# Kernel optimization log

Measured on AMD Instinct MI355X. Metric: run time of the kernel, lower is better.

## Reference

```python
import jax, jax.numpy as jnp
import numpy as np

B, T, L, D = 4, 8, 512, 512
H, KD, VD = 8, 64, 64


def setup_inputs() -> dict:
    key = jax.random.key(0)
    ks = jax.random.split(key, 8)
    s = 0.05
    return {
        "queries": jax.random.normal(ks[0], (B, T, L, D), jnp.float32),
        "keys": jax.random.normal(ks[1], (B, T, L, D), jnp.float32),
        "values": jax.random.normal(ks[2], (B, T, L, D), jnp.float32),
        "attn_mask": jnp.ones((1, 1, 1, L, L), jnp.float32),
        "Wq": jax.random.normal(ks[3], (D, H, KD), jnp.float32) * s,
        "Wk": jax.random.normal(ks[4], (D, H, KD), jnp.float32) * s,
        "Wv": jax.random.normal(ks[5], (D, H, VD), jnp.float32) * s,
        "w_head": jax.random.normal(ks[6], (H,), jnp.float32),
        "tau": jnp.ones((1,), jnp.float32),
        "delta": jnp.zeros((1,), jnp.float32),
    }


def reference(queries, keys, values, attn_mask, Wq, Wk, Wv, w_head, tau, delta):
    # Projections: (b,t,l,d) x (d,h,e) -> (b,t,l,h,e)
    Q = jnp.einsum('btld,dhe->btlhe', queries, Wq)
    K = jnp.einsum('btld,dhe->btlhe', keys, Wk)
    V = jnp.einsum('btld,dhe->btlhe', values, Wv)
    scale = 1.0 / jnp.sqrt(jnp.asarray(KD, jnp.float32))
    # Full score tensor (b,t,h,l,s)
    scores = jnp.einsum('btlhe,btshe->bthls', Q, K)
    # de-stationary rescaling, then scale, then multiplicative mask
    scores = (scores * tau[0] + delta[0]) * scale
    scores = scores * attn_mask
    # Dropout(attn_dropout) before softmax is identity at inference
    p = jax.nn.softmax(scores, axis=-1)
    attn = jnp.einsum('bthls,btshe->bthle', p, V)
    # Per-head scalar weighted sum over heads: (b,t,h,l,e),(h)->(b,t,l,e)
    return jnp.einsum('bthle,h->btle', attn, w_head)
```

## Files before the change

### kernel.cpp

```cpp
#include <hip/hip_runtime.h>
#include <hip/hip_bf16.h>

typedef __bf16 bf16;
typedef __bf16 bf16x4 __attribute__((ext_vector_type(4)));
typedef __bf16 bf16x8 __attribute__((ext_vector_type(8)));
typedef float f32x4 __attribute__((ext_vector_type(4)));
typedef _Float16 half4 __attribute__((ext_vector_type(4)));


#if __has_builtin(__builtin_amdgcn_exp2f)
#define EXP2(x) __builtin_amdgcn_exp2f(x)
#else
#define EXP2(x) exp2f(x)
#endif

static __device__ __forceinline__ f32x4 mfma16(bf16x4 a, bf16x4 b, f32x4 c) {
#if __has_builtin(__builtin_amdgcn_mfma_f32_16x16x16bf16_1k)
    return __builtin_amdgcn_mfma_f32_16x16x16bf16_1k(a, b, c, 0, 0, 0);
#else
    asm("v_mfma_f32_16x16x16_bf16 %0, %1, %2, %0" : "+v"(c) : "v"(a), "v"(b));
    return c;
#endif
}

__global__ __launch_bounds__(256) void prep_kernel(const float* __restrict__ W0,
                                                   const float* __restrict__ W1,
                                                   const float* __restrict__ W2,
                                                   const float* __restrict__ maskf,
                                                   bf16* __restrict__ Wt,
                                                   bf16* __restrict__ Mp) {
    if (blockIdx.z == 3) {
        const int bid = blockIdx.y * 8 + blockIdx.x;
        const int t0 = bid * 256 + threadIdx.x;
        const float4* m4 = (const float4*)maskf;
#pragma unroll
        for (int j = 0; j < 4; ++j) {
            int idx = t0 + j * 16384;
            int q = idx >> 7;
            int sc = idx & 127;
            int cc = sc >> 4;
            int ns = (sc >> 2) & 3;
            int qd = sc & 3;
            float4 v = m4[idx];
            bf16x4 o;
            o[0] = (bf16)v.x; o[1] = (bf16)v.y; o[2] = (bf16)v.z; o[3] = (bf16)v.w;
            size_t off = ((((size_t)(q >> 4) * 8 + cc) * 4 + ns) * 4 + qd) * 64 +
                         (q & 15) * 4;
            *(bf16x4*)&Mp[off] = o;
        }
        return;
    }
    __shared__ float t[64][65];
    const float* W = (blockIdx.z == 0) ? W0 : (blockIdx.z == 1) ? W1 : W2;
    bf16* O = Wt + (size_t)blockIdx.z * 512 * 512;
    const int d0 = blockIdx.x * 64, n0 = blockIdx.y * 64;
    {
        int nl = threadIdx.x & 63, dg = threadIdx.x >> 6;
#pragma unroll
        for (int j = 0; j < 16; ++j) {
            int dl = dg + j * 4;
            t[nl][dl] = W[(size_t)(d0 + dl) * 512 + n0 + nl];
        }
    }
    __syncthreads();
    {
        int dl = threadIdx.x & 63, ng = threadIdx.x >> 6;
#pragma unroll
        for (int j = 0; j < 16; ++j) {
            int nl = ng + j * 4;
            O[(size_t)(n0 + nl) * 512 + d0 + dl] = (bf16)t[nl][dl];
        }
    }
}

__global__ __launch_bounds__(256) void proj_kernel(
    const float* __restrict__ Xq, const float* __restrict__ Xk,
    const float* __restrict__ Xv, const bf16* __restrict__ Wt,
    bf16* __restrict__ Qw, bf16* __restrict__ Kw, bf16* __restrict__ Vt) {
    __shared__ __align__(16) bf16 smem[18432];
    bf16* la = smem;
    bf16* lb = smem + 128 * 72;

    const float* X = (blockIdx.z == 0) ? Xq : (blockIdx.z == 1) ? Xk : Xv;
    const bf16* W  = Wt + (size_t)blockIdx.z * 512 * 512;
    bf16* Out      = (blockIdx.z == 0) ? Qw : (blockIdx.z == 1) ? Kw : Vt;

    const int tid = threadIdx.x, wave = tid >> 6, lane = tid & 63;
    const int quad = lane >> 4, lc = lane & 15;
    const int wm = wave & 1, wn = wave >> 1;
    const int bid = blockIdx.x + (blockIdx.y << 7);
    const int jj = bid >> 3;
    const int yy = jj & 3;
    const int xt = (bid & 7) * 16 + (jj >> 2);
    const int m0 = xt * 128, n0 = yy * 128;

    f32x4 acc[4][4];
#pragma unroll
    for (int ms = 0; ms < 4; ++ms)
#pragma unroll
        for (int ns = 0; ns < 4; ++ns) acc[ms][ns] = (f32x4){0.f, 0.f, 0.f, 0.f};

    const int ar = tid >> 4, ac = tid & 15;
    const int br = tid >> 3, bc = tid & 7;

    float4 xr[8];
    bf16x8 wr[4];
#pragma unroll
    for (int i = 0; i < 8; ++i)
        xr[i] = *(const float4*)&X[(size_t)(m0 + ar + i * 16) * 512 + ac * 4];
#pragma unroll
    for (int i = 0; i < 4; ++i)
        wr[i] = *(const bf16x8*)&W[(size_t)(n0 + br + i * 32) * 512 + bc * 8];

    for (int kb = 0; kb < 512; kb += 64) {
        __syncthreads();
#pragma unroll
        for (int i = 0; i < 8; ++i) {
            float4 x = xr[i];
            bf16x4 p;
            p[0] = (bf16)x.x; p[1] = (bf16)x.y; p[2] = (bf16)x.z; p[3] = (bf16)x.w;
            *(bf16x4*)&la[(ar + i * 16) * 72 + ac * 4] = p;
        }
#pragma unroll
        for (int i = 0; i < 4; ++i)
            *(bf16x8*)&lb[(br + i * 32) * 72 + bc * 8] = wr[i];
        __syncthreads();
        if (kb < 448) {
            int kn = kb + 64;
#pragma unroll
            for (int i = 0; i < 8; ++i)
                xr[i] = *(const float4*)&X[(size_t)(m0 + ar + i * 16) * 512 + kn + ac * 4];
#pragma unroll
            for (int i = 0; i < 4; ++i)
                wr[i] = *(const bf16x8*)&W[(size_t)(n0 + br + i * 32) * 512 + kn + bc * 8];
        }
#pragma unroll
        for (int kk = 0; kk < 2; ++kk) {
            bf16x8 af[4], bfr[4];
#pragma unroll
            for (int ms = 0; ms < 4; ++ms)
                af[ms] = *(bf16x8*)&la[(wm * 64 + ms * 16 + lc) * 72 + kk * 32 + quad * 8];
#pragma unroll
            for (int ns = 0; ns < 4; ++ns)
                bfr[ns] = *(bf16x8*)&lb[(wn * 64 + ns * 16 + lc) * 72 + kk * 32 + quad * 8];
#pragma unroll
            for (int ms = 0; ms < 4; ++ms)
#pragma unroll
                for (int ns = 0; ns < 4; ++ns)
                    acc[ms][ns] = __builtin_amdgcn_mfma_f32_16x16x32_bf16(
                        af[ms], bfr[ns], acc[ms][ns], 0, 0, 0);
        }
    }
    __syncthreads();
    bf16* lds_c = smem;
    if (blockIdx.z != 2) {
#pragma unroll
        for (int ms = 0; ms < 4; ++ms)
#pragma unroll
            for (int ns = 0; ns < 4; ++ns)
#pragma unroll
                for (int r = 0; r < 4; ++r)
                    lds_c[(wm * 64 + ms * 16 + quad * 4 + r) * 136 +
                          wn * 64 + ns * 16 + lc] = (bf16)acc[ms][ns][r];
    } else {
#pragma unroll
        for (int ms = 0; ms < 4; ++ms)
#pragma unroll
            for (int ns = 0; ns < 4; ++ns)
#pragma unroll
                for (int r = 0; r < 4; ++r)
                    lds_c[(wn * 64 + ns * 16 + lc) * 136 +
                          wm * 64 + ms * 16 + quad * 4 + r] = (bf16)acc[ms][ns][r];
    }
    __syncthreads();
    const int bt = m0 >> 9, l0 = m0 & 511;
    if (blockIdx.z != 2) {
        const int ec = tid & 7, rg = tid >> 3;
#pragma unroll
        for (int hc = 0; hc < 2; ++hc) {
            int h = (n0 >> 6) + hc;
#pragma unroll
            for (int p = 0; p < 4; ++p) {
                int row = rg + p * 32;
                bf16x8 v = *(bf16x8*)&lds_c[row * 136 + hc * 64 + ec * 8];
                *(bf16x8*)&Out[(((size_t)bt * 8 + h) * 512 + l0 + row) * 64 + ec * 8] = v;
            }
        }
    } else {
        const int rowp = lane >> 2, cc = lane & 3;
#pragma unroll
        for (int pr = 0; pr < 2; ++pr) {
            int row = wave * 32 + pr * 16 + rowp;
            int h = (n0 >> 6) + (row >> 6);
            int e = row & 63;
            bf16* dst = Out + (((size_t)bt * 8 + h) * 64 + e) * 512 + l0;
#pragma unroll
            for (int pc = 0; pc < 4; ++pc) {
                int mc = cc + pc * 4;
                *(bf16x8*)&dst[mc * 8] = *(bf16x8*)&lds_c[row * 136 + mc * 8];
            }
        }
    }
}

__global__ __launch_bounds__(256, 4) void attn_kernel(
    const bf16* __restrict__ Qw, const bf16* __restrict__ Kw,
    const bf16* __restrict__ Vt, const bf16* __restrict__ Mp,
    const float* __restrict__ w_head, const float* __restrict__ tau,
    const float* __restrict__ delta, float* __restrict__ out,
    void* __restrict__ opart, int mode) {
    __shared__ __align__(16) bf16 lds_k[2][64 * 72];
    __shared__ __align__(16) bf16 lds_vt[2][64 * 72];

    const int tid  = threadIdx.x;
    const int wave = tid >> 6;
    const int lane = tid & 63;
    const int quad = lane >> 4;
    const int lc   = lane & 15;
    const int b    = blockIdx.x;
    const int bth  = b & 255;
    const int qquad = b >> 8;
    const int bt   = bth >> 3;
    const int h    = bth & 7;

    const bf16* Qh  = Qw + (size_t)bth * (512 * 64);
    const bf16* Kh  = Kw + (size_t)bth * (512 * 64);
    const bf16* VtH = Vt + (size_t)bth * (512 * 64);

    const float L2E = 1.4426950408889634f;
    const float ts = tau[0] * 0.125f * L2E;
    const float ds = delta[0] * 0.125f * L2E;
    const float wh = w_head[h];

    const int q0 = qquad * 128 + wave * 32;
    const size_t mbA = (size_t)(q0 >> 4) * 8192 + lane * 4;
    const size_t mbB = mbA + 8192;

    bf16x8 qfA[2], qfB[2];
#pragma unroll
    for (int kk = 0; kk < 2; ++kk) {
        qfA[kk] = *(const bf16x8*)&Qh[(size_t)(q0 + lc) * 64 + kk * 32 + quad * 8];
        qfB[kk] = *(const bf16x8*)&Qh[(size_t)(q0 + 16 + lc) * 64 + kk * 32 + quad * 8];
    }

    f32x4 oA[4], oB[4];
#pragma unroll
    for (int ns = 0; ns < 4; ++ns) {
        oA[ns] = (f32x4){0.f, 0.f, 0.f, 0.f};
        oB[ns] = (f32x4){0.f, 0.f, 0.f, 0.f};
    }
    float lA = 0.f, lB = 0.f;

    const int srow = tid >> 3, scc = tid & 7;
    bf16x8 kr[2], vr[2];
    kr[0] = *(const bf16x8*)&Kh[(size_t)srow * 64 + scc * 8];
    kr[1] = *(const bf16x8*)&Kh[(size_t)(srow + 32) * 64 + scc * 8];
    vr[0] = *(const bf16x8*)&VtH[(size_t)srow * 512 + scc * 8];
    vr[1] = *(const bf16x8*)&VtH[(size_t)(srow + 32) * 512 + scc * 8];
    *(bf16x8*)&lds_k[0][srow * 72 + scc * 8] = kr[0];
    *(bf16x8*)&lds_k[0][(srow + 32) * 72 + scc * 8] = kr[1];
    *(bf16x8*)&lds_vt[0][srow * 72 + scc * 8] = vr[0];
    *(bf16x8*)&lds_vt[0][(srow + 32) * 72 + scc * 8] = vr[1];
    kr[0] = *(const bf16x8*)&Kh[(size_t)(64 + srow) * 64 + scc * 8];
    kr[1] = *(const bf16x8*)&Kh[(size_t)(64 + srow + 32) * 64 + scc * 8];
    vr[0] = *(const bf16x8*)&VtH[(size_t)srow * 512 + 64 + scc * 8];
    vr[1] = *(const bf16x8*)&VtH[(size_t)(srow + 32) * 512 + 64 + scc * 8];

    for (int c = 0; c < 8; ++c) {
        const int buf = c & 1;
        __syncthreads();
        bf16x4 mA[4], mB[4];
        {
            const size_t mc = mbA + (size_t)c * 1024;
            const size_t md = mbB + (size_t)c * 1024;
#pragma unroll
            for (int ns = 0; ns < 4; ++ns) {
                mA[ns] = *(const bf16x4*)&Mp[mc + ns * 256];
                mB[ns] = *(const bf16x4*)&Mp[md + ns * 256];
            }
        }
        f32x4 stA[4], stB[4];
#pragma unroll
        for (int ns = 0; ns < 4; ++ns) {
            stA[ns] = (f32x4){0.f, 0.f, 0.f, 0.f};
            stB[ns] = (f32x4){0.f, 0.f, 0.f, 0.f};
        }
#pragma unroll
        for (int kk = 0; kk < 2; ++kk)
#pragma unroll
            for (int ns = 0; ns < 4; ++ns) {
                bf16x8 ka = *(bf16x8*)&lds_k[buf][(ns * 16 + lc) * 72 + kk * 32 + quad * 8];
                stA[ns] = __builtin_amdgcn_mfma_f32_16x16x32_bf16(ka, qfA[kk], stA[ns], 0, 0, 0);
                stB[ns] = __builtin_amdgcn_mfma_f32_16x16x32_bf16(ka, qfB[kk], stB[ns], 0, 0, 0);
            }
        if (c < 7) {
            const int nb = buf ^ 1;
            *(bf16x8*)&lds_k[nb][srow * 72 + scc * 8] = kr[0];
            *(bf16x8*)&lds_k[nb][(srow + 32) * 72 + scc * 8] = kr[1];
            *(bf16x8*)&lds_vt[nb][srow * 72 + scc * 8] = vr[0];
            *(bf16x8*)&lds_vt[nb][(srow + 32) * 72 + scc * 8] = vr[1];
            if (c < 6) {
                const int s0n = (c + 2) * 64;
                kr[0] = *(const bf16x8*)&Kh[(size_t)(s0n + srow) * 64 + scc * 8];
                kr[1] = *(const bf16x8*)&Kh[(size_t)(s0n + srow + 32) * 64 + scc * 8];
                vr[0] = *(const bf16x8*)&VtH[(size_t)srow * 512 + s0n + scc * 8];
                vr[1] = *(const bf16x8*)&VtH[(size_t)(srow + 32) * 512 + s0n + scc * 8];
            }
        }
        bf16x4 paA[4], paB[4];
#pragma unroll
        for (int ns = 0; ns < 4; ++ns) {
#pragma unroll
            for (int r = 0; r < 4; ++r) {
                float eA = (stA[ns][r] * ts + ds) * (float)mA[ns][r];
                float eB = (stB[ns][r] * ts + ds) * (float)mB[ns][r];
                float pA = EXP2(eA);
                float pB = EXP2(eB);
                lA += pA; lB += pB;
                paA[ns][r] = (bf16)pA;
                paB[ns][r] = (bf16)pB;
            }
        }
#pragma unroll
        for (int ks = 0; ks < 4; ++ks)
#pragma unroll
            for (int ns = 0; ns < 4; ++ns) {
                bf16x4 vv = *(bf16x4*)&lds_vt[buf][(ns * 16 + lc) * 72 + ks * 16 + quad * 4];
                oA[ns] = mfma16(paA[ks], vv, oA[ns]);
                oB[ns] = mfma16(paB[ks], vv, oB[ns]);
            }
    }
    lA += __shfl_xor(lA, 16, 64);
    lA += __shfl_xor(lA, 32, 64);
    lB += __shfl_xor(lB, 16, 64);
    lB += __shfl_xor(lB, 32, 64);
#pragma unroll
    for (int r = 0; r < 4; ++r) {
        float lrA = __shfl(lA, quad * 4 + r, 64);
        float lrB = __shfl(lB, quad * 4 + r, 64);
        float ivA = wh / lrA, ivB = wh / lrB;
        int qqA = q0 + quad * 4 + r;
        int qqB = q0 + 16 + quad * 4 + r;
        if (mode == 0) {
#pragma unroll
            for (int ns = 0; ns < 4; ++ns) {
                int e = ns * 16 + lc;
                atomicAdd(&out[((size_t)bt * 512 + qqA) * 64 + e], oA[ns][r] * ivA);
                atomicAdd(&out[((size_t)bt * 512 + qqB) * 64 + e], oB[ns][r] * ivB);
            }
        } else if (mode == 1) {
            float* op = (float*)opart;
#pragma unroll
            for (int ns = 0; ns < 4; ++ns) {
                int e = ns * 16 + lc;
                op[((size_t)bth * 512 + qqA) * 64 + e] = oA[ns][r] * ivA;
                op[((size_t)bth * 512 + qqB) * 64 + e] = oB[ns][r] * ivB;
            }
        } else {
            _Float16* op = (_Float16*)opart;
#pragma unroll
            for (int ns = 0; ns < 4; ++ns) {
                int e = ns * 16 + lc;
                op[((size_t)bth * 512 + qqA) * 64 + e] = (_Float16)(oA[ns][r] * ivA);
                op[((size_t)bth * 512 + qqB) * 64 + e] = (_Float16)(oB[ns][r] * ivB);
            }
        }
    }
}

__global__ __launch_bounds__(256) void reduce_kernel(const void* __restrict__ part,
                                                     float* __restrict__ out,
                                                     int mode) {
    const int idx = blockIdx.x * 256 + threadIdx.x;
    const int bt = idx >> 13;
    const int rf = idx & 8191;
    f32x4 s = (f32x4){0.f, 0.f, 0.f, 0.f};
    if (mode == 1) {
        const f32x4* p = (const f32x4*)part + (size_t)bt * 65536 + rf;
#pragma unroll
        for (int h = 0; h < 8; ++h) s += p[(size_t)h * 8192];
    } else {
        const half4* p = (const half4*)part + (size_t)bt * 65536 + rf;
#pragma unroll
        for (int h = 0; h < 8; ++h) {
            half4 v = p[(size_t)h * 8192];
            s[0] += (float)v[0]; s[1] += (float)v[1];
            s[2] += (float)v[2]; s[3] += (float)v[3];
        }
    }
    *(f32x4*)&out[(size_t)idx * 4] = s;
}

extern "C" void kernel_launch(void* const* d_in, const int* in_sizes, int n_in,
                              void* d_out, int out_size, void* d_ws, size_t ws_size,
                              hipStream_t stream) {
    const float* queries = (const float*)d_in[0];
    const float* keys    = (const float*)d_in[1];
    const float* values  = (const float*)d_in[2];
    const float* mask    = (const float*)d_in[3];
    const float* Wq      = (const float*)d_in[4];
    const float* Wk      = (const float*)d_in[5];
    const float* Wv      = (const float*)d_in[6];
    const float* w_head  = (const float*)d_in[7];
    const float* tau     = (const float*)d_in[8];
    const float* delta   = (const float*)d_in[9];

    char* ws = (char*)d_ws;
    bf16* Qw = (bf16*)(ws);
    bf16* Kw = (bf16*)(ws + 16777216ull);
    bf16* Vt = (bf16*)(ws + 33554432ull);
    bf16* Wt = (bf16*)(ws + 50331648ull);
    bf16* Mp = (bf16*)(ws + 51904512ull);
    char* Op = ws + 52428800ull;

    int mode = (ws_size >= 52428800ull + 33554432ull) ? 1
             : (ws_size >= 52428800ull + 16777216ull) ? 2 : 0;

    if (mode == 0)
        hipMemsetAsync(d_out, 0, (size_t)out_size * sizeof(float), stream);

    prep_kernel<<<dim3(8, 8, 4), 256, 0, stream>>>(Wq, Wk, Wv, mask, Wt, Mp);

    proj_kernel<<<dim3(128, 4, 3), 256, 0, stream>>>(queries, keys, values, Wt,
                                                     Qw, Kw, Vt);

    attn_kernel<<<1024, 256, 0, stream>>>(Qw, Kw, Vt, Mp, w_head, tau, delta,
                                          (float*)d_out, (void*)Op, mode);

    if (mode != 0)
        reduce_kernel<<<1024, 256, 0, stream>>>((const void*)Op, (float*)d_out,
                                                mode);
}
```

Measured before the change: 224.6 us.

## Double-buffer projection LDS, raise MFMA wave priority, and prefer mode 2 reduction

The projection GEMM now uses two LDS buffers, so the next k-chunk is converted and stored while the current one is consumed. This drops one barrier per iteration at the cost of doubling shared memory to 72 KB, which may lower occupancy. The attention kernel wraps its MFMA blocks in s_setprio to favour matrix issue across waves. The host no longer picks mode 1 and uses mode 2 partial-buffer reduction whenever the workspace allows, which changes the output reduction path.

```diff
diff --git a/kernel.cpp b/kernel.cpp
--- a/kernel.cpp
+++ b/kernel.cpp
@@ -77,9 +77,7 @@
     const float* __restrict__ Xq, const float* __restrict__ Xk,
     const float* __restrict__ Xv, const bf16* __restrict__ Wt,
     bf16* __restrict__ Qw, bf16* __restrict__ Kw, bf16* __restrict__ Vt) {
-    __shared__ __align__(16) bf16 smem[18432];
-    bf16* la = smem;
-    bf16* lb = smem + 128 * 72;
+    __shared__ __align__(16) bf16 smem[36864];
 
     const float* X = (blockIdx.z == 0) ? Xq : (blockIdx.z == 1) ? Xk : Xv;
     const bf16* W  = Wt + (size_t)blockIdx.z * 512 * 512;
@@ -111,28 +109,50 @@
 #pragma unroll
     for (int i = 0; i < 4; ++i)
         wr[i] = *(const bf16x8*)&W[(size_t)(n0 + br + i * 32) * 512 + bc * 8];
-
-    for (int kb = 0; kb < 512; kb += 64) {
+#pragma unroll
+    for (int i = 0; i < 8; ++i) {
+        float4 x = xr[i];
+        bf16x4 p;
+        p[0] = (bf16)x.x; p[1] = (bf16)x.y; p[2] = (bf16)x.z; p[3] = (bf16)x.w;
+        *(bf16x4*)&smem[(ar + i * 16) * 72 + ac * 4] = p;
+    }
+#pragma unroll
+    for (int i = 0; i < 4; ++i)
+        *(bf16x8*)&smem[9216 + (br + i * 32) * 72 + bc * 8] = wr[i];
+#pragma unroll
+    for (int i = 0; i < 8; ++i)
+        xr[i] = *(const float4*)&X[(size_t)(m0 + ar + i * 16) * 512 + 64 + ac * 4];
+#pragma unroll
+    for (int i = 0; i < 4; ++i)
+        wr[i] = *(const bf16x8*)&W[(size_t)(n0 + br + i * 32) * 512 + 64 + bc * 8];
+
+    for (int c = 0; c < 8; ++c) {
+        const int buf = c & 1;
+        bf16* la = smem + buf * 18432;
+        bf16* lb = la + 9216;
         __syncthreads();
-#pragma unroll
-        for (int i = 0; i < 8; ++i) {
-            float4 x = xr[i];
-            bf16x4 p;
-            p[0] = (bf16)x.x; p[1] = (bf16)x.y; p[2] = (bf16)x.z; p[3] = (bf16)x.w;
-            *(bf16x4*)&la[(ar + i * 16) * 72 + ac * 4] = p;
-        }
-#pragma unroll
-        for (int i = 0; i < 4; ++i)
-            *(bf16x8*)&lb[(br + i * 32) * 72 + bc * 8] = wr[i];
-        __syncthreads();
-        if (kb < 448) {
-            int kn = kb + 64;
-#pragma unroll
-            for (int i = 0; i < 8; ++i)
-                xr[i] = *(const float4*)&X[(size_t)(m0 + ar + i * 16) * 512 + kn + ac * 4];
+        if (c < 7) {
+            bf16* lan = smem + (buf ^ 1) * 18432;
+            bf16* lbn = lan + 9216;
+#pragma unroll
+            for (int i = 0; i < 8; ++i) {
+                float4 x = xr[i];
+                bf16x4 p;
+                p[0] = (bf16)x.x; p[1] = (bf16)x.y; p[2] = (bf16)x.z; p[3] = (bf16)x.w;
+                *(bf16x4*)&lan[(ar + i * 16) * 72 + ac * 4] = p;
+            }
 #pragma unroll
             for (int i = 0; i < 4; ++i)
-                wr[i] = *(const bf16x8*)&W[(size_t)(n0 + br + i * 32) * 512 + kn + bc * 8];
+                *(bf16x8*)&lbn[(br + i * 32) * 72 + bc * 8] = wr[i];
+            if (c < 6) {
+                const int kn = (c + 2) * 64;
+#pragma unroll
+                for (int i = 0; i < 8; ++i)
+                    xr[i] = *(const float4*)&X[(size_t)(m0 + ar + i * 16) * 512 + kn + ac * 4];
+#pragma unroll
+                for (int i = 0; i < 4; ++i)
+                    wr[i] = *(const bf16x8*)&W[(size_t)(n0 + br + i * 32) * 512 + kn + bc * 8];
+            }
         }
 #pragma unroll
         for (int kk = 0; kk < 2; ++kk) {
@@ -285,6 +305,7 @@
             stA[ns] = (f32x4){0.f, 0.f, 0.f, 0.f};
             stB[ns] = (f32x4){0.f, 0.f, 0.f, 0.f};
         }
+        __builtin_amdgcn_s_setprio(1);
 #pragma unroll
         for (int kk = 0; kk < 2; ++kk)
 #pragma unroll
@@ -293,6 +314,7 @@
                 stA[ns] = __builtin_amdgcn_mfma_f32_16x16x32_bf16(ka, qfA[kk], stA[ns], 0, 0, 0);
                 stB[ns] = __builtin_amdgcn_mfma_f32_16x16x32_bf16(ka, qfB[kk], stB[ns], 0, 0, 0);
             }
+        __builtin_amdgcn_s_setprio(0);
         if (c < 7) {
             const int nb = buf ^ 1;
             *(bf16x8*)&lds_k[nb][srow * 72 + scc * 8] = kr[0];
@@ -321,6 +343,7 @@
                 paB[ns][r] = (bf16)pB;
             }
         }
+        __builtin_amdgcn_s_setprio(1);
 #pragma unroll
         for (int ks = 0; ks < 4; ++ks)
 #pragma unroll
@@ -329,6 +352,7 @@
                 oA[ns] = mfma16(paA[ks], vv, oA[ns]);
                 oB[ns] = mfma16(paB[ks], vv, oB[ns]);
             }
+        __builtin_amdgcn_s_setprio(0);
     }
     lA += __shfl_xor(lA, 16, 64);
     lA += __shfl_xor(lA, 32, 64);
@@ -413,8 +437,8 @@
     bf16* Mp = (bf16*)(ws + 51904512ull);
     char* Op = ws + 52428800ull;
 
-    int mode = (ws_size >= 52428800ull + 33554432ull) ? 1
-             : (ws_size >= 52428800ull + 16777216ull) ? 2 : 0;
+    int mode = (ws_size >= 52428800ull + 16777216ull) ? 2
+             : 0;
 
     if (mode == 0)
         hipMemsetAsync(d_out, 0, (size_t)out_size * sizeof(float), stream);
```

New measurement: 237.0 us. 1.05x slower.
